# Kernel tuning notes

Measured on AMD Instinct MI355X. Metric: run time of the kernel, lower is better.

The kernel has to match this reference:

```python
import jax, jax.numpy as jnp
import numpy as np

NU, NM = 100000, 20000   # users, merchants
FU, FM = 64, 32          # input feature dims
H = 128                  # hidden_channels
E = 1000000              # edges per edge type
ET = 500000              # target edges


def setup_inputs() -> dict:
    key = jax.random.key(0)
    ks = jax.random.split(key, 24)
    f = lambda i, shape: jax.random.normal(ks[i], shape, jnp.float32) * 0.05
    ri = lambda i, n, hi: jax.random.randint(ks[i], (n,), 0, hi)
    return {
        'x_user': f(0, (NU, FU)),
        'x_merchant': f(1, (NM, FM)),
        'row_um': ri(2, E, NU), 'col_um': ri(3, E, NM),
        'row_mu': ri(4, E, NM), 'col_mu': ri(5, E, NU),
        'row_t': ri(6, ET, NU), 'col_t': ri(7, ET, NM),
        'W1l_um': f(8, (FU, H)), 'W1r_um': f(9, (FM, H)), 'b1_um': jnp.zeros((H,), jnp.float32),
        'W1l_mu': f(10, (FM, H)), 'W1r_mu': f(11, (FU, H)), 'b1_mu': jnp.zeros((H,), jnp.float32),
        'W2l_um': f(12, (H, H)), 'W2r_um': f(13, (H, H)), 'b2_um': jnp.zeros((H,), jnp.float32),
        'W2l_mu': f(14, (H, H)), 'W2r_mu': f(15, (H, H)), 'b2_mu': jnp.zeros((H,), jnp.float32),
        'Wc1': f(16, (2 * H, H)), 'bc1': jnp.zeros((H,), jnp.float32),
        'Wc2': f(17, (H, 1)), 'bc2': jnp.zeros((1,), jnp.float32),
    }


def _sage(x_src, x_dst, row, col, Wl, Wr, b, n_dst):
    # PyG SAGEConv (aggr='mean'): lin_l(mean of neighbor msgs) + lin_r(root) + bias
    deg = jax.ops.segment_sum(jnp.ones(row.shape[0], x_src.dtype), col, num_segments=n_dst)
    agg = jax.ops.segment_sum(x_src[row], col, num_segments=n_dst)
    agg = agg / jnp.maximum(deg, 1.0)[:, None]
    return agg @ Wl + x_dst @ Wr + b


def reference(x_user, x_merchant, row_um, col_um, row_mu, col_mu, row_t, col_t,
              W1l_um, W1r_um, b1_um, W1l_mu, W1r_mu, b1_mu,
              W2l_um, W2r_um, b2_um, W2l_mu, W2r_mu, b2_mu,
              Wc1, bc1, Wc2, bc2):
    # Layer 1 (each dest type receives exactly one edge type -> hetero-mean is identity)
    h_m = jax.nn.relu(_sage(x_user, x_merchant, row_um, col_um, W1l_um, W1r_um, b1_um, NM))
    h_u = jax.nn.relu(_sage(x_merchant, x_user, row_mu, col_mu, W1l_mu, W1r_mu, b1_mu, NU))
    # Layer 2 (no activation)
    z_m = _sage(h_u, h_m, row_um, col_um, W2l_um, W2r_um, b2_um, NM)
    z_u = _sage(h_m, h_u, row_mu, col_mu, W2l_mu, W2r_mu, b2_mu, NU)
    # Edge classifier: gather sender ('user') / receiver ('merchant'), concat, MLP
    z = jnp.concatenate([z_u[row_t], z_m[col_t]], axis=-1)  # [ET, 2H]
    h = jax.nn.relu(z @ Wc1 + bc1)
    return (h @ Wc2 + bc2).reshape(-1)
```

## Files before the change

### kernel.cpp

```cpp
#include <hip/hip_runtime.h>
#include <hip/hip_bf16.h>

#define NUV 100000
#define NMV 20000
#define NEV 1000000
#define ETV 500000

#define CHK 8192
#define NCH 123
#define WNM 5000
#define WNU 25000
#define NCA 5
#define NCB 25
#define HGRID 1954
#define MBLK 5000
#define G1TM 313
#define G2MB 313

typedef unsigned short u16;
typedef unsigned int u32;
typedef __attribute__((ext_vector_type(8))) short s16x8;
typedef __attribute__((ext_vector_type(4))) float f32x4;
typedef __attribute__((ext_vector_type(2))) unsigned int u32x2;
typedef __attribute__((ext_vector_type(4))) unsigned int u32x4;

__device__ inline u16 bf16r(float f) {
  u32 b = __builtin_bit_cast(u32, f);
  u32 r = b + 0x7fffu + ((b >> 16) & 1u);
  return (u16)(r >> 16);
}
__device__ inline float bflo(u32 v) { return __builtin_bit_cast(float, v << 16); }
__device__ inline float bfhi(u32 v) { return __builtin_bit_cast(float, v & 0xffff0000u); }

#define GLOAD_LDS16(src, dst) \
  __builtin_amdgcn_global_load_lds((const __attribute__((address_space(1))) void*)(src), \
                                   (__attribute__((address_space(3))) void*)(dst), 16, 0, 0)

__global__ __launch_bounds__(512) void k_hist_lds(
    const int* __restrict__ col_um, u32* __restrict__ rankp_um, u32* __restrict__ cnt_um,
    const int* __restrict__ col_mu, u32* __restrict__ rankp_mu, u32* __restrict__ cnt_mu) {
  __shared__ u32 hist[WNU];
  int bid = blockIdx.x, tid = threadIdx.x;
  bool um = bid < NCH;
  const int* col = um ? col_um : col_mu;
  u32* rankp = um ? rankp_um : rankp_mu;
  u32* cntp = um ? cnt_um : cnt_mu;
  int Wn = um ? WNM : WNU;
  int blk = um ? bid : bid - NCH;
  int e0 = blk * CHK;
  for (int i = tid; i < Wn; i += 512) hist[i] = 0;
  __syncthreads();
  #pragma unroll
  for (int it = 0; it < CHK / 2048; ++it) {
    int li = e0 + (it * 512 + tid) * 4;
    if (li < NEV) {
      int4 c = *(const int4*)(col + li);
      int cc[4] = {c.x, c.y, c.z, c.w};
      u32 pk = 0;
      #pragma unroll
      for (int q = 0; q < 4; ++q) {
        int d = cc[q];
        int sh = 8 * (d & 3);
        u32 old = atomicAdd(&hist[d >> 2], 1u << sh);
        pk |= ((old >> sh) & 0xFFu) << (8 * q);
      }
      rankp[li >> 2] = pk;
    }
  }
  __syncthreads();
  u32* dst = cntp + (size_t)blk * Wn;
  for (int i = tid; i < Wn; i += 512) dst[i] = hist[i];
}

__global__ __launch_bounds__(1024) void k_scan_s1(
    const u32* __restrict__ cnt_um, u32* __restrict__ pre_um,
    const u32* __restrict__ cnt_mu, u32* __restrict__ pre_mu,
    int* __restrict__ T, int* __restrict__ bsum) {
  int b = blockIdx.x;
  const u32* cnt; u32* pre; int Wn; int w0; int* Tout;
  if (b < NCA) { cnt = cnt_um; pre = pre_um; Wn = WNM; w0 = b * 1024; Tout = T; }
  else         { cnt = cnt_mu; pre = pre_mu; Wn = WNU; w0 = (b - NCA) * 1024; Tout = T + NMV; }
  __shared__ int wsum[16];
  int tid = threadIdx.x, lane = tid & 63, w = tid >> 6;
  int wd = w0 + tid;
  int r0 = 0, r1 = 0, r2 = 0, r3 = 0;
  if (wd < Wn) {
    #pragma unroll 4
    for (int bb = 0; bb < NCH; ++bb) {
      u32 v = cnt[(size_t)bb * Wn + wd];
      pre[(size_t)bb * Wn + wd] =
          (u32)r0 | ((u32)r1 << 8) | ((u32)r2 << 16) | ((u32)r3 << 24);
      r0 += v & 0xFF; r1 += (v >> 8) & 0xFF; r2 += (v >> 16) & 0xFF; r3 += (v >> 24) & 0xFF;
    }
    *(int4*)(Tout + wd * 4) = make_int4(r0, r1, r2, r3);
  }
  int tot = r0 + r1 + r2 + r3;
  #pragma unroll
  for (int d = 1; d < 64; d <<= 1) tot += __shfl_xor(tot, d);
  if (lane == 0) wsum[w] = tot;
  __syncthreads();
  if (tid == 0) {
    int a = 0;
    #pragma unroll
    for (int j = 0; j < 16; ++j) a += wsum[j];
    bsum[b] = a;
  }
}

__global__ __launch_bounds__(128) void k_scan_s2(int* __restrict__ bsum,
                                                 int* __restrict__ off_um, int* __restrict__ off_mu) {
  int tid = threadIdx.x;
  int wv = tid >> 6, lane = tid & 63;
  if (wv == 0) {
    int v = (lane < NCA) ? bsum[lane] : 0;
    int s = v;
    #pragma unroll
    for (int d = 1; d < 64; d <<= 1) { int t = __shfl_up(s, d); if (lane >= d) s += t; }
    if (lane < NCA) bsum[lane] = s - v;
  } else {
    int v = (lane < NCB) ? bsum[NCA + lane] : 0;
    int s = v;
    #pragma unroll
    for (int d = 1; d < 64; d <<= 1) { int t = __shfl_up(s, d); if (lane >= d) s += t; }
    if (lane < NCB) bsum[NCA + lane] = s - v;
  }
  if (tid == 0) { off_um[NMV] = NEV; off_mu[NUV] = NEV; }
}

__global__ __launch_bounds__(1024) void k_scan_s3(int* __restrict__ off_um,
                                                  int* __restrict__ off_mu,
                                                  const int* __restrict__ T,
                                                  const int* __restrict__ bsum) {
  int b = blockIdx.x;
  int N; int c0; int* offo; const int* Tin;
  if (b < NCA) { N = NMV; c0 = b * 4096; offo = off_um; Tin = T; }
  else         { N = NUV; c0 = (b - NCA) * 4096; offo = off_mu; Tin = T + NMV; }
  int carry = bsum[b];
  __shared__ int wsum[16];
  int tid = threadIdx.x, lane = tid & 63, w = tid >> 6;
  int c = c0 + tid * 4;
  int4 tv = make_int4(0, 0, 0, 0);
  if (c < N) tv = *(const int4*)(Tin + c);
  int p1 = tv.x + tv.y, p2 = p1 + tv.z, p3 = p2 + tv.w;
  int sc = p3;
  #pragma unroll
  for (int d = 1; d < 64; d <<= 1) { int t = __shfl_up(sc, d); if (lane >= d) sc += t; }
  if (lane == 63) wsum[w] = sc;
  __syncthreads();
  if (w == 0 && lane < 16) {
    int ws_ = wsum[lane];
    #pragma unroll
    for (int d = 1; d < 16; d <<= 1) { int t = __shfl_up(ws_, d, 16); if (lane >= d) ws_ += t; }
    wsum[lane] = ws_;
  }
  __syncthreads();
  int ex = sc - p3 + (w ? wsum[w - 1] : 0) + carry;
  if (c < N) *(int4*)(offo + c) = make_int4(ex, ex + tv.x, ex + p1, ex + p2);
}

__global__ __launch_bounds__(256) void k_scatter3(
    const int* __restrict__ col_um, const int* __restrict__ row_um,
    const u32* __restrict__ rankp_um, const u32* __restrict__ pre_um,
    const int* __restrict__ off_um, int* __restrict__ srow_um,
    const int* __restrict__ col_mu, const int* __restrict__ row_mu,
    const u32* __restrict__ rankp_mu, const u32* __restrict__ pre_mu,
    const int* __restrict__ off_mu, int* __restrict__ srow_mu) {
  int i = (blockIdx.x * 256 + threadIdx.x) * 4;
  if (i >= 2 * NEV) return;
  bool um = i < NEV;
  const int* col = um ? col_um : col_mu;
  const int* row = um ? row_um : row_mu;
  const u32* rankp = um ? rankp_um : rankp_mu;
  const u32* pre = um ? pre_um : pre_mu;
  const int* off = um ? off_um : off_mu;
  int Wn = um ? WNM : WNU;
  int* srow = um ? srow_um : srow_mu;
  int lo = um ? i : i - NEV;
  int blk = lo >> 13;
  const u32* prep = pre + (size_t)blk * Wn;
  int4 c = *(const int4*)(col + lo);
  int4 rr = *(const int4*)(row + lo);
  u32 pk = rankp[lo >> 2];
  int cc[4] = {c.x, c.y, c.z, c.w}, rv[4] = {rr.x, rr.y, rr.z, rr.w};
  #pragma unroll
  for (int q = 0; q < 4; ++q) {
    int d = cc[q];
    int prefix = (int)((prep[d >> 2] >> (8 * (d & 3))) & 0xFF);
    int rank = (int)((pk >> (8 * q)) & 0xFF);
    srow[off[d] + prefix + rank] = rv[q];
  }
}

__global__ __launch_bounds__(256) void k_prep_w(
    const float* __restrict__ W1l_um, const float* __restrict__ W1r_um,
    const float* __restrict__ W1l_mu, const float* __restrict__ W1r_mu,
    const float* __restrict__ W2l_um, const float* __restrict__ W2r_um,
    const float* __restrict__ W2l_mu, const float* __restrict__ W2r_mu,
    const float* __restrict__ b2_um, const float* __restrict__ b2_mu,
    const float* __restrict__ Wc1, const float* __restrict__ bc1,
    u16* __restrict__ WtA_u, u16* __restrict__ WtB_u,
    u16* __restrict__ WtA_m, u16* __restrict__ WtB_m,
    u16* __restrict__ Wt1_m, u16* __restrict__ Wt1_u,
    float* __restrict__ bias_u, float* __restrict__ bias_m) {
  int t = blockIdx.x * 256 + threadIdx.x;
  if (t < 65536) {
    int mat = t >> 14, rem = t & 16383;
    int o = rem >> 7, k = rem & 127;
    const float* W2 = mat == 0 ? W2l_mu : mat == 1 ? W2r_mu : mat == 2 ? W2l_um : W2r_um;
    const float* wc = Wc1 + (mat >= 2 ? 128 * 128 : 0) + o;
    float s = 0.f;
    #pragma unroll 4
    for (int j = 0; j < 128; ++j) s += W2[k * 128 + j] * wc[j * 128];
    u16* dst = mat == 0 ? WtA_u : mat == 1 ? WtB_u : mat == 2 ? WtA_m : WtB_m;
    dst[o * 128 + k] = bf16r(s);
  } else if (t < 65536 + 256) {
    int r = t - 65536;
    int o = r & 127;
    if (r < 128) {
      float s = 0.f;
      for (int j = 0; j < 128; ++j) s += b2_mu[j] * Wc1[j * 128 + o];
      bias_u[o] = s;
    } else {
      float s = bc1[o];
      for (int j = 0; j < 128; ++j) s += b2_um[j] * Wc1[(128 + j) * 128 + o];
      bias_m[o] = s;
    }
  } else if (t < 65792 + 32768) {
    int idx = t - 65792;
    int mat = idx >> 14, rem = idx & 16383;
    int o = rem >> 7, k = rem & 127;
    if (mat == 0) {
      float v = k < 64 ? W1l_um[k * 128 + o] : (k < 96 ? W1r_um[(k - 64) * 128 + o] : 0.f);
      Wt1_m[o * 128 + k] = bf16r(v);
    } else {
      float v = k < 32 ? W1l_mu[k * 128 + o] : (k < 96 ? W1r_mu[(k - 32) * 128 + o] : 0.f);
      Wt1_u[o * 128 + k] = bf16r(v);
    }
  }
}

__global__ __launch_bounds__(256) void k_prep_x(
    const float* __restrict__ x_user, const float* __restrict__ x_merch,
    u32* __restrict__ cat_u, u32* __restrict__ cat_m) {
  int id = blockIdx.x * 256 + threadIdx.x;
  if (id < NUV * 12) {
    int row = id / 12, wg = id % 12;
    if (wg < 8) {
      const float* src = x_user + (size_t)row * 64 + wg * 8;
      float4 a = *(const float4*)src, b = *(const float4*)(src + 4);
      u32x4 r;
      r[0] = (u32)bf16r(a.x) | ((u32)bf16r(a.y) << 16);
      r[1] = (u32)bf16r(a.z) | ((u32)bf16r(a.w) << 16);
      r[2] = (u32)bf16r(b.x) | ((u32)bf16r(b.y) << 16);
      r[3] = (u32)bf16r(b.z) | ((u32)bf16r(b.w) << 16);
      *(u32x4*)(cat_u + (size_t)row * 64 + 16 + wg * 4) = r;
    } else {
      *(u32x4*)(cat_u + (size_t)row * 64 + 48 + (wg - 8) * 4) = (u32x4){0, 0, 0, 0};
    }
  } else if (id < NUV * 12 + NMV * 8) {
    int id2 = id - NUV * 12;
    int row = id2 / 8, wg = id2 % 8;
    if (wg < 4) {
      const float* src = x_merch + (size_t)row * 32 + wg * 8;
      float4 a = *(const float4*)src, b = *(const float4*)(src + 4);
      u32x4 r;
      r[0] = (u32)bf16r(a.x) | ((u32)bf16r(a.y) << 16);
      r[1] = (u32)bf16r(a.z) | ((u32)bf16r(a.w) << 16);
      r[2] = (u32)bf16r(b.x) | ((u32)bf16r(b.y) << 16);
      r[3] = (u32)bf16r(b.z) | ((u32)bf16r(b.w) << 16);
      *(u32x4*)(cat_m + (size_t)row * 64 + 32 + wg * 4) = r;
    } else {
      *(u32x4*)(cat_m + (size_t)row * 64 + 48 + (wg - 4) * 4) = (u32x4){0, 0, 0, 0};
    }
  }
}

__global__ __launch_bounds__(256) void k_agg_l1(
    const int* __restrict__ off_um, const int* __restrict__ srow_um,
    const int* __restrict__ off_mu, const int* __restrict__ srow_mu,
    u32* __restrict__ cat_u, u32* __restrict__ cat_m) {
  int bid = blockIdx.x, tid = threadIdx.x;
  int l = tid & 63, g = l >> 3, lr = l & 7;
  if (bid < MBLK) {
    int wid = (bid * 256 + tid) >> 6;
    int s = off_um[wid], t = off_um[wid + 1];
    const u32* gx = cat_u;
    float a[8] = {};
    int j = s;
    for (; j + 32 <= t; j += 32) {
      int r0 = srow_um[j + g], r1 = srow_um[j + 8 + g];
      int r2 = srow_um[j + 16 + g], r3 = srow_um[j + 24 + g];
      u32x4 v0 = *(const u32x4*)(gx + (size_t)r0 * 64 + 16 + lr * 4);
      u32x4 v1 = *(const u32x4*)(gx + (size_t)r1 * 64 + 16 + lr * 4);
      u32x4 v2 = *(const u32x4*)(gx + (size_t)r2 * 64 + 16 + lr * 4);
      u32x4 v3 = *(const u32x4*)(gx + (size_t)r3 * 64 + 16 + lr * 4);
      #pragma unroll
      for (int k = 0; k < 4; ++k) {
        a[2 * k] += (bflo(v0[k]) + bflo(v1[k])) + (bflo(v2[k]) + bflo(v3[k]));
        a[2 * k + 1] += (bfhi(v0[k]) + bfhi(v1[k])) + (bfhi(v2[k]) + bfhi(v3[k]));
      }
    }
    for (; j + 8 <= t; j += 8) {
      int r0 = srow_um[j + g];
      u32x4 v0 = *(const u32x4*)(gx + (size_t)r0 * 64 + 16 + lr * 4);
      #pragma unroll
      for (int k = 0; k < 4; ++k) { a[2 * k] += bflo(v0[k]); a[2 * k + 1] += bfhi(v0[k]); }
    }
    if (g < t - j) {
      int r0 = srow_um[j + g];
      u32x4 v0 = *(const u32x4*)(gx + (size_t)r0 * 64 + 16 + lr * 4);
      #pragma unroll
      for (int k = 0; k < 4; ++k) { a[2 * k] += bflo(v0[k]); a[2 * k + 1] += bfhi(v0[k]); }
    }
    #pragma unroll
    for (int k = 0; k < 8; ++k) {
      a[k] += __shfl_xor(a[k], 8);
      a[k] += __shfl_xor(a[k], 16);
      a[k] += __shfl_xor(a[k], 32);
    }
    if (g == 0) {
      float inv = 1.f / (float)max(t - s, 1);
      u32x4 o;
      #pragma unroll
      for (int k = 0; k < 4; ++k)
        o[k] = (u32)bf16r(a[2 * k] * inv) | ((u32)bf16r(a[2 * k + 1] * inv) << 16);
      *(u32x4*)(cat_m + (size_t)wid * 64 + lr * 4) = o;
    }
  } else {
    int wid = ((bid - MBLK) * 256 + tid) >> 6;
    int s = off_mu[wid], t = off_mu[wid + 1];
    const u32* gx = cat_m;
    float a[4] = {};
    int j = s;
    for (; j + 32 <= t; j += 32) {
      int r0 = srow_mu[j + g], r1 = srow_mu[j + 8 + g];
      int r2 = srow_mu[j + 16 + g], r3 = srow_mu[j + 24 + g];
      u32x2 v0 = *(const u32x2*)(gx + (size_t)r0 * 64 + 32 + lr * 2);
      u32x2 v1 = *(const u32x2*)(gx + (size_t)r1 * 64 + 32 + lr * 2);
      u32x2 v2 = *(const u32x2*)(gx + (size_t)r2 * 64 + 32 + lr * 2);
      u32x2 v3 = *(const u32x2*)(gx + (size_t)r3 * 64 + 32 + lr * 2);
      #pragma unroll
      for (int k = 0; k < 2; ++k) {
        a[2 * k] += (bflo(v0[k]) + bflo(v1[k])) + (bflo(v2[k]) + bflo(v3[k]));
        a[2 * k + 1] += (bfhi(v0[k]) + bfhi(v1[k])) + (bfhi(v2[k]) + bfhi(v3[k]));
      }
    }
    for (; j + 8 <= t; j += 8) {
      int r0 = srow_mu[j + g];
      u32x2 v0 = *(const u32x2*)(gx + (size_t)r0 * 64 + 32 + lr * 2);
      #pragma unroll
      for (int k = 0; k < 2; ++k) { a[2 * k] += bflo(v0[k]); a[2 * k + 1] += bfhi(v0[k]); }
    }
    if (g < t - j) {
      int r0 = srow_mu[j + g];
      u32x2 v0 = *(const u32x2*)(gx + (size_t)r0 * 64 + 32 + lr * 2);
      #pragma unroll
      for (int k = 0; k < 2; ++k) { a[2 * k] += bflo(v0[k]); a[2 * k + 1] += bfhi(v0[k]); }
    }
    #pragma unroll
    for (int k = 0; k < 4; ++k) {
      a[k] += __shfl_xor(a[k], 8);
      a[k] += __shfl_xor(a[k], 16);
      a[k] += __shfl_xor(a[k], 32);
    }
    if (g == 0) {
      float inv = 1.f / (float)max(t - s, 1);
      u32x2 o;
      #pragma unroll
      for (int k = 0; k < 2; ++k)
        o[k] = (u32)bf16r(a[2 * k] * inv) | ((u32)bf16r(a[2 * k + 1] * inv) << 16);
      *(u32x2*)(cat_u + (size_t)wid * 64 + lr * 2) = o;
    }
  }
}

__global__ __launch_bounds__(256) void k_gemm1_mfma(
    const u16* __restrict__ cat_m, const u16* __restrict__ Wt1_m,
    const float* __restrict__ b1_um, u16* __restrict__ h_m,
    const u16* __restrict__ cat_u, const u16* __restrict__ Wt1_u,
    const float* __restrict__ b1_mu, u16* __restrict__ h_u) {
  __shared__ u16 Zs[64 * 128];
  int tid = threadIdx.x, bid = blockIdx.x;
  const u16 *cat, *Wt; const float* bias; u16* ho; int nd, r0;
  if (bid < G1TM) { cat = cat_m; Wt = Wt1_m; bias = b1_um; ho = h_m; nd = NMV; r0 = bid * 64; }
  else { cat = cat_u; Wt = Wt1_u; bias = b1_mu; ho = h_u; nd = NUV; r0 = (bid - G1TM) * 64; }
  #pragma unroll
  for (int it = 0; it < 4; ++it) {
    int q = tid + it * 256;
    int rl = q >> 4;
    int cc = (q & 15) ^ (rl & 7);
    int r = r0 + rl; r = r < nd ? r : nd - 1;
    const u16* src = cat + (size_t)r * 128 + cc * 8;
    u16* dst = Zs + (tid >> 6) * 512 + it * 2048;
    GLOAD_LDS16(src, dst);
  }
  __syncthreads();
  int l = tid & 63, wv = tid >> 6;
  int lg = l >> 4, lr = l & 15;
  f32x4 acc[4][2];
  #pragma unroll
  for (int mt = 0; mt < 4; ++mt)
    #pragma unroll
    for (int c = 0; c < 2; ++c) acc[mt][c] = (f32x4){0.f, 0.f, 0.f, 0.f};
  #pragma unroll
  for (int cti = 0; cti < 2; ++cti) {
    int o = (wv * 2 + cti) * 16 + lr;
    const u16* wp = Wt + (size_t)o * 128 + lg * 8;
    s16x8 b[4];
    #pragma unroll
    for (int ks = 0; ks < 4; ++ks) b[ks] = *(const s16x8*)(wp + ks * 32);
    #pragma unroll
    for (int mt = 0; mt < 4; ++mt) {
      int rl = mt * 16 + lr;
      int rb = rl * 256, sw = (rl & 7) << 4;
      #pragma unroll
      for (int ks = 0; ks < 4; ++ks) {
        s16x8 a = *(const s16x8*)((const char*)Zs + ((rb + ks * 64 + lg * 16) ^ sw));
        acc[mt][cti] = __builtin_amdgcn_mfma_f32_16x16x32_bf16(a, b[ks], acc[mt][cti], 0, 0, 0);
      }
    }
  }
  float bv[2];
  #pragma unroll
  for (int cti = 0; cti < 2; ++cti) bv[cti] = bias[(wv * 2 + cti) * 16 + lr];
  #pragma unroll
  for (int mt = 0; mt < 4; ++mt)
    #pragma unroll
    for (int cti = 0; cti < 2; ++cti) {
      int o = (wv * 2 + cti) * 16 + lr;
      #pragma unroll
      for (int rg = 0; rg < 4; ++rg) {
        int r = r0 + mt * 16 + lg * 4 + rg;
        if (r < nd) {
          float v = acc[mt][cti][rg] + bv[cti];
          v = v > 0.f ? v : 0.f;
          ho[(size_t)r * 128 + o] = bf16r(v);
        }
      }
    }
}

__global__ __launch_bounds__(256) void k_agg_l2(
    const int* __restrict__ off_um, const int* __restrict__ srow_um,
    const u16* __restrict__ h_u, u16* __restrict__ aggb_m,
    const int* __restrict__ off_mu, const int* __restrict__ srow_mu,
    const u16* __restrict__ h_m, u16* __restrict__ aggb_u) {
  int bid = blockIdx.x, tid = threadIdx.x;
  const int* off; const int* srow; const u32* x; u32* ag; int wid;
  if (bid < MBLK) {
    off = off_um; srow = srow_um; x = (const u32*)h_u; ag = (u32*)aggb_m;
    wid = (bid * 256 + tid) >> 6;
  } else {
    off = off_mu; srow = srow_mu; x = (const u32*)h_m; ag = (u32*)aggb_u;
    wid = ((bid - MBLK) * 256 + tid) >> 6;
  }
  int l = tid & 63, g = l >> 4, lr = l & 15;
  int s = off[wid], t = off[wid + 1];
  float a[8] = {};
  int j = s;
  for (; j + 16 <= t; j += 16) {
    int r0 = srow[j + g], r1 = srow[j + 4 + g];
    int r2 = srow[j + 8 + g], r3 = srow[j + 12 + g];
    u32x4 v0 = *(const u32x4*)(x + (size_t)r0 * 64 + lr * 4);
    u32x4 v1 = *(const u32x4*)(x + (size_t)r1 * 64 + lr * 4);
    u32x4 v2 = *(const u32x4*)(x + (size_t)r2 * 64 + lr * 4);
    u32x4 v3 = *(const u32x4*)(x + (size_t)r3 * 64 + lr * 4);
    #pragma unroll
    for (int k = 0; k < 4; ++k) {
      a[2 * k] += (bflo(v0[k]) + bflo(v1[k])) + (bflo(v2[k]) + bflo(v3[k]));
      a[2 * k + 1] += (bfhi(v0[k]) + bfhi(v1[k])) + (bfhi(v2[k]) + bfhi(v3[k]));
    }
  }
  for (; j + 4 <= t; j += 4) {
    int r0 = srow[j + g];
    u32x4 v0 = *(const u32x4*)(x + (size_t)r0 * 64 + lr * 4);
    #pragma unroll
    for (int k = 0; k < 4; ++k) { a[2 * k] += bflo(v0[k]); a[2 * k + 1] += bfhi(v0[k]); }
  }
  if (g < t - j) {
    int r0 = srow[j + g];
    u32x4 v0 = *(const u32x4*)(x + (size_t)r0 * 64 + lr * 4);
    #pragma unroll
    for (int k = 0; k < 4; ++k) { a[2 * k] += bflo(v0[k]); a[2 * k + 1] += bfhi(v0[k]); }
  }
  #pragma unroll
  for (int k = 0; k < 8; ++k) {
    a[k] += __shfl_xor(a[k], 16);
    a[k] += __shfl_xor(a[k], 32);
  }
  if (g == 0) {
    float inv = 1.f / (float)max(t - s, 1);
    u32x4 o;
    #pragma unroll
    for (int k = 0; k < 4; ++k)
      o[k] = (u32)bf16r(a[2 * k] * inv) | ((u32)bf16r(a[2 * k + 1] * inv) << 16);
    *(u32x4*)(ag + (size_t)wid * 64 + lr * 4) = o;
  }
}

__global__ __launch_bounds__(256) void k_gemm2_mfma(
    const u16* __restrict__ aggb_m, const u16* __restrict__ h_m,
    const u16* __restrict__ WtA_m, const u16* __restrict__ WtB_m,
    const float* __restrict__ bias_m, u16* __restrict__ pm_b,
    const u16* __restrict__ aggb_u, const u16* __restrict__ h_u,
    const u16* __restrict__ WtA_u, const u16* __restrict__ WtB_u,
    const float* __restrict__ bias_u, u16* __restrict__ pu_b) {
  __shared__ u16 Zs[64 * 256];
  int tid = threadIdx.x;
  int bid = blockIdx.x;
  const u16 *aggb, *hb, *Wtl, *Wtr; const float* bias; u16* zb; int nd, r0;
  if (bid < G2MB) {
    aggb = aggb_m; hb = h_m; Wtl = WtA_m; Wtr = WtB_m; bias = bias_m; zb = pm_b;
    nd = NMV; r0 = bid * 64;
  } else {
    aggb = aggb_u; hb = h_u; Wtl = WtA_u; Wtr = WtB_u; bias = bias_u; zb = pu_b;
    nd = NUV; r0 = (bid - G2MB) * 64;
  }
  {
    int half = (tid >> 4) & 1;
    const u16* tab = half ? hb : aggb;
    #pragma unroll
    for (int it = 0; it < 8; ++it) {
      int q = tid + it * 256;
      int rl = q >> 5;
      int cc = (q & 15) ^ (rl & 7);
      int r = r0 + rl; r = r < nd ? r : nd - 1;
      const u16* src = tab + (size_t)r * 128 + cc * 8;
      u16* dst = Zs + (tid >> 6) * 512 + it * 2048;
      GLOAD_LDS16(src, dst);
    }
  }
  __syncthreads();
  int l = tid & 63, wv = tid >> 6;
  int lg = l >> 4, lr = l & 15;
  f32x4 acc[4][2];
  #pragma unroll
  for (int mt = 0; mt < 4; ++mt)
    #pragma unroll
    for (int c = 0; c < 2; ++c) acc[mt][c] = (f32x4){0.f, 0.f, 0.f, 0.f};
  #pragma unroll
  for (int cti = 0; cti < 2; ++cti) {
    int o = (wv * 2 + cti) * 16 + lr;
    const u16* wpl = Wtl + (size_t)o * 128 + lg * 8;
    const u16* wpr = Wtr + (size_t)o * 128 + lg * 8;
    s16x8 b[8];
    #pragma unroll
    for (int ks = 0; ks < 4; ++ks) b[ks] = *(const s16x8*)(wpl + ks * 32);
    #pragma unroll
    for (int ks = 0; ks < 4; ++ks) b[ks + 4] = *(const s16x8*)(wpr + ks * 32);
    #pragma unroll
    for (int mt = 0; mt < 4; ++mt) {
      int rl = mt * 16 + lr;
      int rb = rl * 512, sw = (rl & 7) << 4;
      #pragma unroll
      for (int ks = 0; ks < 8; ++ks) {
        s16x8 a = *(const s16x8*)((const char*)Zs + ((rb + ks * 64 + lg * 16) ^ sw));
        acc[mt][cti] = __builtin_amdgcn_mfma_f32_16x16x32_bf16(a, b[ks], acc[mt][cti], 0, 0, 0);
      }
    }
  }
  float bv[2];
  #pragma unroll
  for (int cti = 0; cti < 2; ++cti) bv[cti] = bias[(wv * 2 + cti) * 16 + lr];
  #pragma unroll
  for (int mt = 0; mt < 4; ++mt)
    #pragma unroll
    for (int cti = 0; cti < 2; ++cti) {
      int o = (wv * 2 + cti) * 16 + lr;
      #pragma unroll
      for (int rg = 0; rg < 4; ++rg) {
        int r = r0 + mt * 16 + lg * 4 + rg;
        if (r < nd) zb[(size_t)r * 128 + o] = bf16r(acc[mt][cti][rg] + bv[cti]);
      }
    }
}

__global__ __launch_bounds__(256) void k_edge(
    const u32* __restrict__ pu, const u32* __restrict__ pm,
    const int* __restrict__ row_t, const int* __restrict__ col_t,
    const float* __restrict__ Wc2, const float* __restrict__ bc2,
    float* __restrict__ out) {
  __shared__ float res[256];
  int tid = threadIdx.x, l = tid & 63, wv = tid >> 6;
  int lr = l & 15, g = l >> 4;
  float w2v[8];
  #pragma unroll
  for (int q = 0; q < 8; ++q) w2v[q] = Wc2[lr * 8 + q];
  int base = blockIdx.x * 256 + wv * 64;
  #pragma unroll 2
  for (int it = 0; it < 16; ++it) {
    int e = base + it * 4 + g;
    int ec = e < ETV ? e : ETV - 1;
    int r = row_t[ec], c = col_t[ec];
    u32x4 a = *(const u32x4*)(pu + (size_t)r * 64 + lr * 4);
    u32x4 b = *(const u32x4*)(pm + (size_t)c * 64 + lr * 4);
    float p = 0.f;
    #pragma unroll
    for (int q = 0; q < 4; ++q) {
      float h0 = bflo(a[q]) + bflo(b[q]);
      float h1 = bfhi(a[q]) + bfhi(b[q]);
      h0 = h0 > 0.f ? h0 : 0.f;
      h1 = h1 > 0.f ? h1 : 0.f;
      p += h0 * w2v[2 * q] + h1 * w2v[2 * q + 1];
    }
    p += __shfl_xor(p, 1); p += __shfl_xor(p, 2);
    p += __shfl_xor(p, 4); p += __shfl_xor(p, 8);
    if (lr == 0) res[wv * 64 + it * 4 + g] = p;
  }
  __syncthreads();
  int eo = blockIdx.x * 256 + tid;
  if (eo < ETV) out[eo] = res[tid] + bc2[0];
}

extern "C" void kernel_launch(void* const* d_in, const int* in_sizes, int n_in,
                              void* d_out, int out_size, void* d_ws, size_t ws_size,
                              hipStream_t stream) {
  const float* x_user  = (const float*)d_in[0];
  const float* x_merch = (const float*)d_in[1];
  const int* row_um = (const int*)d_in[2]; const int* col_um = (const int*)d_in[3];
  const int* row_mu = (const int*)d_in[4]; const int* col_mu = (const int*)d_in[5];
  const int* row_t  = (const int*)d_in[6]; const int* col_t  = (const int*)d_in[7];
  const float* W1l_um = (const float*)d_in[8];  const float* W1r_um = (const float*)d_in[9];  const float* b1_um = (const float*)d_in[10];
  const float* W1l_mu = (const float*)d_in[11]; const float* W1r_mu = (const float*)d_in[12]; const float* b1_mu = (const float*)d_in[13];
  const float* W2l_um = (const float*)d_in[14]; const float* W2r_um = (const float*)d_in[15]; const float* b2_um = (const float*)d_in[16];
  const float* W2l_mu = (const float*)d_in[17]; const float* W2r_mu = (const float*)d_in[18]; const float* b2_mu = (const float*)d_in[19];
  const float* Wc1 = (const float*)d_in[20]; const float* bc1 = (const float*)d_in[21];
  const float* Wc2 = (const float*)d_in[22]; const float* bc2 = (const float*)d_in[23];
  float* out = (float*)d_out;

  char* ws = (char*)d_ws;
  size_t p = 0;
  auto alloc = [&](size_t bytes) -> char* {
    char* r = ws + p;
    p = (p + bytes + 255) & ~(size_t)255;
    return r;
  };
  u32* cnt_um = (u32*)alloc((size_t)NCH * WNM * 4);
  u32* cnt_mu = (u32*)alloc((size_t)NCH * WNU * 4);
  u32* pre_um = (u32*)alloc((size_t)NCH * WNM * 4);
  u32* pre_mu = (u32*)alloc((size_t)NCH * WNU * 4);
  u32* rankp_um = (u32*)alloc((size_t)(NEV / 4) * 4);
  u32* rankp_mu = (u32*)alloc((size_t)(NEV / 4) * 4);
  int* off_um = (int*)alloc((size_t)(NMV + 4) * 4);
  int* off_mu = (int*)alloc((size_t)(NUV + 4) * 4);
  int* T    = (int*)alloc((size_t)(NMV + NUV) * 4);
  int* bsum = (int*)alloc((size_t)(NCA + NCB) * 4);
  int* srow_um = (int*)alloc((size_t)NEV * 4);
  int* srow_mu = (int*)alloc((size_t)NEV * 4);
  u16* cat_m = (u16*)alloc((size_t)NMV * 128 * 2);
  u16* cat_u = (u16*)alloc((size_t)NUV * 128 * 2);
  u16* h_m   = (u16*)alloc((size_t)NMV * 128 * 2);
  u16* h_u   = (u16*)alloc((size_t)NUV * 128 * 2);
  u16* aggb_m = (u16*)alloc((size_t)NMV * 128 * 2);
  u16* aggb_u = (u16*)alloc((size_t)NUV * 128 * 2);
  u16* pm_b  = (u16*)alloc((size_t)NMV * 128 * 2);
  u16* pu_b  = (u16*)alloc((size_t)NUV * 128 * 2);
  u16* WtA_u = (u16*)alloc((size_t)128 * 128 * 2);
  u16* WtB_u = (u16*)alloc((size_t)128 * 128 * 2);
  u16* WtA_m = (u16*)alloc((size_t)128 * 128 * 2);
  u16* WtB_m = (u16*)alloc((size_t)128 * 128 * 2);
  u16* Wt1_m = (u16*)alloc((size_t)128 * 128 * 2);
  u16* Wt1_u = (u16*)alloc((size_t)128 * 128 * 2);
  float* bias_u = (float*)alloc(128 * 4);
  float* bias_m = (float*)alloc(128 * 4);
  if (p > ws_size) return;

  k_prep_w<<<386, 256, 0, stream>>>(W1l_um, W1r_um, W1l_mu, W1r_mu,
                                    W2l_um, W2r_um, W2l_mu, W2r_mu, b2_um, b2_mu, Wc1, bc1,
                                    WtA_u, WtB_u, WtA_m, WtB_m, Wt1_m, Wt1_u, bias_u, bias_m);
  k_prep_x<<<(NUV * 12 + NMV * 8 + 255) / 256, 256, 0, stream>>>(x_user, x_merch,
                                                                 (u32*)cat_u, (u32*)cat_m);
  k_hist_lds<<<2 * NCH, 512, 0, stream>>>(col_um, rankp_um, cnt_um,
                                          col_mu, rankp_mu, cnt_mu);
  k_scan_s1<<<NCA + NCB, 1024, 0, stream>>>(cnt_um, pre_um, cnt_mu, pre_mu, T, bsum);
  k_scan_s2<<<1, 128, 0, stream>>>(bsum, off_um, off_mu);
  k_scan_s3<<<NCA + NCB, 1024, 0, stream>>>(off_um, off_mu, T, bsum);
  k_scatter3<<<HGRID, 256, 0, stream>>>(col_um, row_um, rankp_um, pre_um, off_um, srow_um,
                                        col_mu, row_mu, rankp_mu, pre_mu, off_mu, srow_mu);
  k_agg_l1<<<MBLK + NUV / 4, 256, 0, stream>>>(off_um, srow_um, off_mu, srow_mu,
                                               (u32*)cat_u, (u32*)cat_m);
  k_gemm1_mfma<<<G1TM + (NUV + 63) / 64, 256, 0, stream>>>(cat_m, Wt1_m, b1_um, h_m,
                                                           cat_u, Wt1_u, b1_mu, h_u);
  k_agg_l2<<<MBLK + NUV / 4, 256, 0, stream>>>(off_um, srow_um, h_u, aggb_m,
                                               off_mu, srow_mu, h_m, aggb_u);
  k_gemm2_mfma<<<G2MB + (NUV + 63) / 64, 256, 0, stream>>>(
      aggb_m, h_m, WtA_m, WtB_m, bias_m, pm_b,
      aggb_u, h_u, WtA_u, WtB_u, bias_u, pu_b);
  k_edge<<<(ETV + 255) / 256, 256, 0, stream>>>((const u32*)pu_b, (const u32*)pm_b,
                                                row_t, col_t, Wc2, bc2, out);
}
```

Measured before the change: 322.5 us.

## Fuse layer-2 mean aggregation into the GEMM and merge prep and scan launches

Layer-2 neighbour mean aggregation now runs inside the layer-2 MFMA GEMM kernel. Each block gathers and averages its 64 destination rows straight into LDS, which removes the aggb intermediate buffers and their global write and read-back. The weight-prep and feature-prep kernels are merged into one launch. The tiny scan_s2 kernel is dropped, and each scan_s3 block now sums the block totals it needs on its own. The cost is far less gather parallelism in the fused kernel: one wave handles 16 rows in sequence instead of one row per wave, so gather latency may be hidden less well.

```diff
diff --git a/kernel.cpp b/kernel.cpp
--- a/kernel.cpp
+++ b/kernel.cpp
@@ -16,6 +16,7 @@
 #define MBLK 5000
 #define G1TM 313
 #define G2MB 313
+#define PWB 386
 
 typedef unsigned short u16;
 typedef unsigned int u32;
@@ -107,26 +108,6 @@
   }
 }
 
-__global__ __launch_bounds__(128) void k_scan_s2(int* __restrict__ bsum,
-                                                 int* __restrict__ off_um, int* __restrict__ off_mu) {
-  int tid = threadIdx.x;
-  int wv = tid >> 6, lane = tid & 63;
-  if (wv == 0) {
-    int v = (lane < NCA) ? bsum[lane] : 0;
-    int s = v;
-    #pragma unroll
-    for (int d = 1; d < 64; d <<= 1) { int t = __shfl_up(s, d); if (lane >= d) s += t; }
-    if (lane < NCA) bsum[lane] = s - v;
-  } else {
-    int v = (lane < NCB) ? bsum[NCA + lane] : 0;
-    int s = v;
-    #pragma unroll
-    for (int d = 1; d < 64; d <<= 1) { int t = __shfl_up(s, d); if (lane >= d) s += t; }
-    if (lane < NCB) bsum[NCA + lane] = s - v;
-  }
-  if (tid == 0) { off_um[NMV] = NEV; off_mu[NUV] = NEV; }
-}
-
 __global__ __launch_bounds__(1024) void k_scan_s3(int* __restrict__ off_um,
                                                   int* __restrict__ off_mu,
                                                   const int* __restrict__ T,
@@ -135,9 +116,18 @@
   int N; int c0; int* offo; const int* Tin;
   if (b < NCA) { N = NMV; c0 = b * 4096; offo = off_um; Tin = T; }
   else         { N = NUV; c0 = (b - NCA) * 4096; offo = off_mu; Tin = T + NMV; }
-  int carry = bsum[b];
+  __shared__ int carry_s;
   __shared__ int wsum[16];
   int tid = threadIdx.x, lane = tid & 63, w = tid >> 6;
+  if (tid == 0) {
+    int lo = (b < NCA) ? 0 : NCA;
+    int c = 0;
+    for (int j = lo; j < b; ++j) c += bsum[j];
+    carry_s = c;
+    if (b == 0) { off_um[NMV] = NEV; off_mu[NUV] = NEV; }
+  }
+  __syncthreads();
+  int carry = carry_s;
   int c = c0 + tid * 4;
   int4 tv = make_int4(0, 0, 0, 0);
   if (c < N) tv = *(const int4*)(Tin + c);
@@ -191,7 +181,8 @@
   }
 }
 
-__global__ __launch_bounds__(256) void k_prep_w(
+__global__ __launch_bounds__(256) void k_prep(
+    const float* __restrict__ x_user, const float* __restrict__ x_merch,
     const float* __restrict__ W1l_um, const float* __restrict__ W1r_um,
     const float* __restrict__ W1l_mu, const float* __restrict__ W1r_mu,
     const float* __restrict__ W2l_um, const float* __restrict__ W2r_um,
@@ -201,76 +192,76 @@
     u16* __restrict__ WtA_u, u16* __restrict__ WtB_u,
     u16* __restrict__ WtA_m, u16* __restrict__ WtB_m,
     u16* __restrict__ Wt1_m, u16* __restrict__ Wt1_u,
-    float* __restrict__ bias_u, float* __restrict__ bias_m) {
-  int t = blockIdx.x * 256 + threadIdx.x;
-  if (t < 65536) {
-    int mat = t >> 14, rem = t & 16383;
-    int o = rem >> 7, k = rem & 127;
-    const float* W2 = mat == 0 ? W2l_mu : mat == 1 ? W2r_mu : mat == 2 ? W2l_um : W2r_um;
-    const float* wc = Wc1 + (mat >= 2 ? 128 * 128 : 0) + o;
-    float s = 0.f;
-    #pragma unroll 4
-    for (int j = 0; j < 128; ++j) s += W2[k * 128 + j] * wc[j * 128];
-    u16* dst = mat == 0 ? WtA_u : mat == 1 ? WtB_u : mat == 2 ? WtA_m : WtB_m;
-    dst[o * 128 + k] = bf16r(s);
-  } else if (t < 65536 + 256) {
-    int r = t - 65536;
-    int o = r & 127;
-    if (r < 128) {
+    float* __restrict__ bias_u, float* __restrict__ bias_m,
+    u32* __restrict__ cat_u, u32* __restrict__ cat_m) {
+  int bid = blockIdx.x;
+  if (bid < PWB) {
+    int t = bid * 256 + threadIdx.x;
+    if (t < 65536) {
+      int mat = t >> 14, rem = t & 16383;
+      int o = rem >> 7, k = rem & 127;
+      const float* W2 = mat == 0 ? W2l_mu : mat == 1 ? W2r_mu : mat == 2 ? W2l_um : W2r_um;
+      const float* wc = Wc1 + (mat >= 2 ? 128 * 128 : 0) + o;
       float s = 0.f;
-      for (int j = 0; j < 128; ++j) s += b2_mu[j] * Wc1[j * 128 + o];
-      bias_u[o] = s;
-    } else {
-      float s = bc1[o];
-      for (int j = 0; j < 128; ++j) s += b2_um[j] * Wc1[(128 + j) * 128 + o];
-      bias_m[o] = s;
-    }
-  } else if (t < 65792 + 32768) {
-    int idx = t - 65792;
-    int mat = idx >> 14, rem = idx & 16383;
-    int o = rem >> 7, k = rem & 127;
-    if (mat == 0) {
-      float v = k < 64 ? W1l_um[k * 128 + o] : (k < 96 ? W1r_um[(k - 64) * 128 + o] : 0.f);
-      Wt1_m[o * 128 + k] = bf16r(v);
-    } else {
-      float v = k < 32 ? W1l_mu[k * 128 + o] : (k < 96 ? W1r_mu[(k - 32) * 128 + o] : 0.f);
-      Wt1_u[o * 128 + k] = bf16r(v);
-    }
-  }
-}
-
-__global__ __launch_bounds__(256) void k_prep_x(
-    const float* __restrict__ x_user, const float* __restrict__ x_merch,
-    u32* __restrict__ cat_u, u32* __restrict__ cat_m) {
-  int id = blockIdx.x * 256 + threadIdx.x;
-  if (id < NUV * 12) {
-    int row = id / 12, wg = id % 12;
-    if (wg < 8) {
-      const float* src = x_user + (size_t)row * 64 + wg * 8;
-      float4 a = *(const float4*)src, b = *(const float4*)(src + 4);
-      u32x4 r;
-      r[0] = (u32)bf16r(a.x) | ((u32)bf16r(a.y) << 16);
-      r[1] = (u32)bf16r(a.z) | ((u32)bf16r(a.w) << 16);
-      r[2] = (u32)bf16r(b.x) | ((u32)bf16r(b.y) << 16);
-      r[3] = (u32)bf16r(b.z) | ((u32)bf16r(b.w) << 16);
-      *(u32x4*)(cat_u + (size_t)row * 64 + 16 + wg * 4) = r;
-    } else {
-      *(u32x4*)(cat_u + (size_t)row * 64 + 48 + (wg - 8) * 4) = (u32x4){0, 0, 0, 0};
-    }
-  } else if (id < NUV * 12 + NMV * 8) {
-    int id2 = id - NUV * 12;
-    int row = id2 / 8, wg = id2 % 8;
-    if (wg < 4) {
-      const float* src = x_merch + (size_t)row * 32 + wg * 8;
-      float4 a = *(const float4*)src, b = *(const float4*)(src + 4);
-      u32x4 r;
-      r[0] = (u32)bf16r(a.x) | ((u32)bf16r(a.y) << 16);
-      r[1] = (u32)bf16r(a.z) | ((u32)bf16r(a.w) << 16);
-      r[2] = (u32)bf16r(b.x) | ((u32)bf16r(b.y) << 16);
-      r[3] = (u32)bf16r(b.z) | ((u32)bf16r(b.w) << 16);
-      *(u32x4*)(cat_m + (size_t)row * 64 + 32 + wg * 4) = r;
-    } else {
-      *(u32x4*)(cat_m + (size_t)row * 64 + 48 + (wg - 4) * 4) = (u32x4){0, 0, 0, 0};
+      #pragma unroll 4
+      for (int j = 0; j < 128; ++j) s += W2[k * 128 + j] * wc[j * 128];
+      u16* dst = mat == 0 ? WtA_u : mat == 1 ? WtB_u : mat == 2 ? WtA_m : WtB_m;
+      dst[o * 128 + k] = bf16r(s);
+    } else if (t < 65536 + 256) {
+      int r = t - 65536;
+      int o = r & 127;
+      if (r < 128) {
+        float s = 0.f;
+        for (int j = 0; j < 128; ++j) s += b2_mu[j] * Wc1[j * 128 + o];
+        bias_u[o] = s;
+      } else {
+        float s = bc1[o];
+        for (int j = 0; j < 128; ++j) s += b2_um[j] * Wc1[(128 + j) * 128 + o];
+        bias_m[o] = s;
+      }
+    } else if (t < 65792 + 32768) {
+      int idx = t - 65792;
+      int mat = idx >> 14, rem = idx & 16383;
+      int o = rem >> 7, k = rem & 127;
+      if (mat == 0) {
+        float v = k < 64 ? W1l_um[k * 128 + o] : (k < 96 ? W1r_um[(k - 64) * 128 + o] : 0.f);
+        Wt1_m[o * 128 + k] = bf16r(v);
+      } else {
+        float v = k < 32 ? W1l_mu[k * 128 + o] : (k < 96 ? W1r_mu[(k - 32) * 128 + o] : 0.f);
+        Wt1_u[o * 128 + k] = bf16r(v);
+      }
+    }
+  } else {
+    int id = (bid - PWB) * 256 + threadIdx.x;
+    if (id < NUV * 12) {
+      int row = id / 12, wg = id % 12;
+      if (wg < 8) {
+        const float* src = x_user + (size_t)row * 64 + wg * 8;
+        float4 a = *(const float4*)src, b = *(const float4*)(src + 4);
+        u32x4 r;
+        r[0] = (u32)bf16r(a.x) | ((u32)bf16r(a.y) << 16);
+        r[1] = (u32)bf16r(a.z) | ((u32)bf16r(a.w) << 16);
+        r[2] = (u32)bf16r(b.x) | ((u32)bf16r(b.y) << 16);
+        r[3] = (u32)bf16r(b.z) | ((u32)bf16r(b.w) << 16);
+        *(u32x4*)(cat_u + (size_t)row * 64 + 16 + wg * 4) = r;
+      } else {
+        *(u32x4*)(cat_u + (size_t)row * 64 + 48 + (wg - 8) * 4) = (u32x4){0, 0, 0, 0};
+      }
+    } else if (id < NUV * 12 + NMV * 8) {
+      int id2 = id - NUV * 12;
+      int row = id2 / 8, wg = id2 % 8;
+      if (wg < 4) {
+        const float* src = x_merch + (size_t)row * 32 + wg * 8;
+        float4 a = *(const float4*)src, b = *(const float4*)(src + 4);
+        u32x4 r;
+        r[0] = (u32)bf16r(a.x) | ((u32)bf16r(a.y) << 16);
+        r[1] = (u32)bf16r(a.z) | ((u32)bf16r(a.w) << 16);
+        r[2] = (u32)bf16r(b.x) | ((u32)bf16r(b.y) << 16);
+        r[3] = (u32)bf16r(b.z) | ((u32)bf16r(b.w) << 16);
+        *(u32x4*)(cat_m + (size_t)row * 64 + 32 + wg * 4) = r;
+      } else {
+        *(u32x4*)(cat_m + (size_t)row * 64 + 48 + (wg - 4) * 4) = (u32x4){0, 0, 0, 0};
+      }
     }
   }
 }
@@ -440,99 +431,85 @@
     }
 }
 
-__global__ __launch_bounds__(256) void k_agg_l2(
+__global__ __launch_bounds__(256) void k_gemm2f(
     const int* __restrict__ off_um, const int* __restrict__ srow_um,
-    const u16* __restrict__ h_u, u16* __restrict__ aggb_m,
     const int* __restrict__ off_mu, const int* __restrict__ srow_mu,
-    const u16* __restrict__ h_m, u16* __restrict__ aggb_u) {
-  int bid = blockIdx.x, tid = threadIdx.x;
-  const int* off; const int* srow; const u32* x; u32* ag; int wid;
-  if (bid < MBLK) {
-    off = off_um; srow = srow_um; x = (const u32*)h_u; ag = (u32*)aggb_m;
-    wid = (bid * 256 + tid) >> 6;
-  } else {
-    off = off_mu; srow = srow_mu; x = (const u32*)h_m; ag = (u32*)aggb_u;
-    wid = ((bid - MBLK) * 256 + tid) >> 6;
-  }
-  int l = tid & 63, g = l >> 4, lr = l & 15;
-  int s = off[wid], t = off[wid + 1];
-  float a[8] = {};
-  int j = s;
-  for (; j + 16 <= t; j += 16) {
-    int r0 = srow[j + g], r1 = srow[j + 4 + g];
-    int r2 = srow[j + 8 + g], r3 = srow[j + 12 + g];
-    u32x4 v0 = *(const u32x4*)(x + (size_t)r0 * 64 + lr * 4);
-    u32x4 v1 = *(const u32x4*)(x + (size_t)r1 * 64 + lr * 4);
-    u32x4 v2 = *(const u32x4*)(x + (size_t)r2 * 64 + lr * 4);
-    u32x4 v3 = *(const u32x4*)(x + (size_t)r3 * 64 + lr * 4);
-    #pragma unroll
-    for (int k = 0; k < 4; ++k) {
-      a[2 * k] += (bflo(v0[k]) + bflo(v1[k])) + (bflo(v2[k]) + bflo(v3[k]));
-      a[2 * k + 1] += (bfhi(v0[k]) + bfhi(v1[k])) + (bfhi(v2[k]) + bfhi(v3[k]));
-    }
-  }
-  for (; j + 4 <= t; j += 4) {
-    int r0 = srow[j + g];
-    u32x4 v0 = *(const u32x4*)(x + (size_t)r0 * 64 + lr * 4);
-    #pragma unroll
-    for (int k = 0; k < 4; ++k) { a[2 * k] += bflo(v0[k]); a[2 * k + 1] += bfhi(v0[k]); }
-  }
-  if (g < t - j) {
-    int r0 = srow[j + g];
-    u32x4 v0 = *(const u32x4*)(x + (size_t)r0 * 64 + lr * 4);
-    #pragma unroll
-    for (int k = 0; k < 4; ++k) { a[2 * k] += bflo(v0[k]); a[2 * k + 1] += bfhi(v0[k]); }
-  }
-  #pragma unroll
-  for (int k = 0; k < 8; ++k) {
-    a[k] += __shfl_xor(a[k], 16);
-    a[k] += __shfl_xor(a[k], 32);
-  }
-  if (g == 0) {
-    float inv = 1.f / (float)max(t - s, 1);
-    u32x4 o;
-    #pragma unroll
-    for (int k = 0; k < 4; ++k)
-      o[k] = (u32)bf16r(a[2 * k] * inv) | ((u32)bf16r(a[2 * k + 1] * inv) << 16);
-    *(u32x4*)(ag + (size_t)wid * 64 + lr * 4) = o;
-  }
-}
-
-__global__ __launch_bounds__(256) void k_gemm2_mfma(
-    const u16* __restrict__ aggb_m, const u16* __restrict__ h_m,
+    const u16* __restrict__ h_m, const u16* __restrict__ h_u,
     const u16* __restrict__ WtA_m, const u16* __restrict__ WtB_m,
     const float* __restrict__ bias_m, u16* __restrict__ pm_b,
-    const u16* __restrict__ aggb_u, const u16* __restrict__ h_u,
     const u16* __restrict__ WtA_u, const u16* __restrict__ WtB_u,
     const float* __restrict__ bias_u, u16* __restrict__ pu_b) {
-  __shared__ u16 Zs[64 * 256];
-  int tid = threadIdx.x;
-  int bid = blockIdx.x;
-  const u16 *aggb, *hb, *Wtl, *Wtr; const float* bias; u16* zb; int nd, r0;
+  __shared__ u16 Zh[64 * 128];
+  __shared__ u16 Za[64 * 128];
+  int tid = threadIdx.x, bid = blockIdx.x;
+  const int *off, *srow; const u32* gtab; const u16 *hb, *Wtl, *Wtr;
+  const float* bias; u16* zb; int nd, r0;
   if (bid < G2MB) {
-    aggb = aggb_m; hb = h_m; Wtl = WtA_m; Wtr = WtB_m; bias = bias_m; zb = pm_b;
-    nd = NMV; r0 = bid * 64;
+    off = off_um; srow = srow_um; gtab = (const u32*)h_u; hb = h_m;
+    Wtl = WtA_m; Wtr = WtB_m; bias = bias_m; zb = pm_b; nd = NMV; r0 = bid * 64;
   } else {
-    aggb = aggb_u; hb = h_u; Wtl = WtA_u; Wtr = WtB_u; bias = bias_u; zb = pu_b;
-    nd = NUV; r0 = (bid - G2MB) * 64;
-  }
-  {
-    int half = (tid >> 4) & 1;
-    const u16* tab = half ? hb : aggb;
-    #pragma unroll
-    for (int it = 0; it < 8; ++it) {
-      int q = tid + it * 256;
-      int rl = q >> 5;
-      int cc = (q & 15) ^ (rl & 7);
-      int r = r0 + rl; r = r < nd ? r : nd - 1;
-      const u16* src = tab + (size_t)r * 128 + cc * 8;
-      u16* dst = Zs + (tid >> 6) * 512 + it * 2048;
-      GLOAD_LDS16(src, dst);
-    }
-  }
-  __syncthreads();
+    off = off_mu; srow = srow_mu; gtab = (const u32*)h_m; hb = h_u;
+    Wtl = WtA_u; Wtr = WtB_u; bias = bias_u; zb = pu_b; nd = NUV; r0 = (bid - G2MB) * 64;
+  }
+  #pragma unroll
+  for (int it = 0; it < 4; ++it) {
+    int q = tid + it * 256;
+    int rl = q >> 4;
+    int cc = (q & 15) ^ (rl & 7);
+    int r = r0 + rl; r = r < nd ? r : nd - 1;
+    GLOAD_LDS16(hb + (size_t)r * 128 + cc * 8, Zh + (tid >> 6) * 512 + it * 2048);
+  }
   int l = tid & 63, wv = tid >> 6;
-  int lg = l >> 4, lr = l & 15;
+  int g = l >> 4, lr = l & 15;
+  for (int i = 0; i < 16; ++i) {
+    int rl = wv * 16 + i;
+    int r = r0 + rl;
+    bool ok = r < nd;
+    int s = ok ? off[r] : 0, t = ok ? off[r + 1] : 0;
+    float a[8] = {};
+    int j = s;
+    for (; j + 16 <= t; j += 16) {
+      int r0e = srow[j + g], r1e = srow[j + 4 + g];
+      int r2e = srow[j + 8 + g], r3e = srow[j + 12 + g];
+      u32x4 v0 = *(const u32x4*)(gtab + (size_t)r0e * 64 + lr * 4);
+      u32x4 v1 = *(const u32x4*)(gtab + (size_t)r1e * 64 + lr * 4);
+      u32x4 v2 = *(const u32x4*)(gtab + (size_t)r2e * 64 + lr * 4);
+      u32x4 v3 = *(const u32x4*)(gtab + (size_t)r3e * 64 + lr * 4);
+      #pragma unroll
+      for (int k = 0; k < 4; ++k) {
+        a[2 * k] += (bflo(v0[k]) + bflo(v1[k])) + (bflo(v2[k]) + bflo(v3[k]));
+        a[2 * k + 1] += (bfhi(v0[k]) + bfhi(v1[k])) + (bfhi(v2[k]) + bfhi(v3[k]));
+      }
+    }
+    for (; j + 4 <= t; j += 4) {
+      int r0e = srow[j + g];
+      u32x4 v0 = *(const u32x4*)(gtab + (size_t)r0e * 64 + lr * 4);
+      #pragma unroll
+      for (int k = 0; k < 4; ++k) { a[2 * k] += bflo(v0[k]); a[2 * k + 1] += bfhi(v0[k]); }
+    }
+    if (g < t - j) {
+      int r0e = srow[j + g];
+      u32x4 v0 = *(const u32x4*)(gtab + (size_t)r0e * 64 + lr * 4);
+      #pragma unroll
+      for (int k = 0; k < 4; ++k) { a[2 * k] += bflo(v0[k]); a[2 * k + 1] += bfhi(v0[k]); }
+    }
+    #pragma unroll
+    for (int k = 0; k < 8; ++k) {
+      a[k] += __shfl_xor(a[k], 16);
+      a[k] += __shfl_xor(a[k], 32);
+    }
+    if (g == 0) {
+      float inv = 1.f / (float)max(t - s, 1);
+      u32x4 o;
+      #pragma unroll
+      for (int k = 0; k < 4; ++k)
+        o[k] = ok ? ((u32)bf16r(a[2 * k] * inv) | ((u32)bf16r(a[2 * k + 1] * inv) << 16)) : 0u;
+      int byt = (rl * 256 + lr * 16) ^ ((rl & 7) << 4);
+      *(u32x4*)((char*)Za + byt) = o;
+    }
+  }
+  __syncthreads();
+  int lg = g;
   f32x4 acc[4][2];
   #pragma unroll
   for (int mt = 0; mt < 4; ++mt)
@@ -551,11 +528,16 @@
     #pragma unroll
     for (int mt = 0; mt < 4; ++mt) {
       int rl = mt * 16 + lr;
-      int rb = rl * 512, sw = (rl & 7) << 4;
-      #pragma unroll
-      for (int ks = 0; ks < 8; ++ks) {
-        s16x8 a = *(const s16x8*)((const char*)Zs + ((rb + ks * 64 + lg * 16) ^ sw));
+      int rb = rl * 256, sw = (rl & 7) << 4;
+      #pragma unroll
+      for (int ks = 0; ks < 4; ++ks) {
+        s16x8 a = *(const s16x8*)((const char*)Za + ((rb + ks * 64 + lg * 16) ^ sw));
         acc[mt][cti] = __builtin_amdgcn_mfma_f32_16x16x32_bf16(a, b[ks], acc[mt][cti], 0, 0, 0);
+      }
+      #pragma unroll
+      for (int ks = 0; ks < 4; ++ks) {
+        s16x8 a = *(const s16x8*)((const char*)Zh + ((rb + ks * 64 + lg * 16) ^ sw));
+        acc[mt][cti] = __builtin_amdgcn_mfma_f32_16x16x32_bf16(a, b[ks + 4], acc[mt][cti], 0, 0, 0);
       }
     }
   }
@@ -651,8 +633,6 @@
   u16* cat_u = (u16*)alloc((size_t)NUV * 128 * 2);
   u16* h_m   = (u16*)alloc((size_t)NMV * 128 * 2);
   u16* h_u   = (u16*)alloc((size_t)NUV * 128 * 2);
-  u16* aggb_m = (u16*)alloc((size_t)NMV * 128 * 2);
-  u16* aggb_u = (u16*)alloc((size_t)NUV * 128 * 2);
   u16* pm_b  = (u16*)alloc((size_t)NMV * 128 * 2);
   u16* pu_b  = (u16*)alloc((size_t)NUV * 128 * 2);
   u16* WtA_u = (u16*)alloc((size_t)128 * 128 * 2);
@@ -665,15 +645,14 @@
   float* bias_m = (float*)alloc(128 * 4);
   if (p > ws_size) return;
 
-  k_prep_w<<<386, 256, 0, stream>>>(W1l_um, W1r_um, W1l_mu, W1r_mu,
-                                    W2l_um, W2r_um, W2l_mu, W2r_mu, b2_um, b2_mu, Wc1, bc1,
-                                    WtA_u, WtB_u, WtA_m, WtB_m, Wt1_m, Wt1_u, bias_u, bias_m);
-  k_prep_x<<<(NUV * 12 + NMV * 8 + 255) / 256, 256, 0, stream>>>(x_user, x_merch,
-                                                                 (u32*)cat_u, (u32*)cat_m);
+  k_prep<<<PWB + (NUV * 12 + NMV * 8 + 255) / 256, 256, 0, stream>>>(
+      x_user, x_merch, W1l_um, W1r_um, W1l_mu, W1r_mu,
+      W2l_um, W2r_um, W2l_mu, W2r_mu, b2_um, b2_mu, Wc1, bc1,
+      WtA_u, WtB_u, WtA_m, WtB_m, Wt1_m, Wt1_u, bias_u, bias_m,
+      (u32*)cat_u, (u32*)cat_m);
   k_hist_lds<<<2 * NCH, 512, 0, stream>>>(col_um, rankp_um, cnt_um,
                                           col_mu, rankp_mu, cnt_mu);
   k_scan_s1<<<NCA + NCB, 1024, 0, stream>>>(cnt_um, pre_um, cnt_mu, pre_mu, T, bsum);
-  k_scan_s2<<<1, 128, 0, stream>>>(bsum, off_um, off_mu);
   k_scan_s3<<<NCA + NCB, 1024, 0, stream>>>(off_um, off_mu, T, bsum);
   k_scatter3<<<HGRID, 256, 0, stream>>>(col_um, row_um, rankp_um, pre_um, off_um, srow_um,
                                         col_mu, row_mu, rankp_mu, pre_mu, off_mu, srow_mu);
@@ -681,11 +660,9 @@
                                                (u32*)cat_u, (u32*)cat_m);
   k_gemm1_mfma<<<G1TM + (NUV + 63) / 64, 256, 0, stream>>>(cat_m, Wt1_m, b1_um, h_m,
                                                            cat_u, Wt1_u, b1_mu, h_u);
-  k_agg_l2<<<MBLK + NUV / 4, 256, 0, stream>>>(off_um, srow_um, h_u, aggb_m,
-                                               off_mu, srow_mu, h_m, aggb_u);
-  k_gemm2_mfma<<<G2MB + (NUV + 63) / 64, 256, 0, stream>>>(
-      aggb_m, h_m, WtA_m, WtB_m, bias_m, pm_b,
-      aggb_u, h_u, WtA_u, WtB_u, bias_u, pu_b);
+  k_gemm2f<<<G2MB + (NUV + 63) / 64, 256, 0, stream>>>(
+      off_um, srow_um, off_mu, srow_mu, h_m, h_u,
+      WtA_m, WtB_m, bias_m, pm_b, WtA_u, WtB_u, bias_u, pu_b);
   k_edge<<<(ETV + 255) / 256, 256, 0, stream>>>((const u32*)pu_b, (const u32*)pm_b,
                                                 row_t, col_t, Wc2, bc2, out);
 }
```

Measured after the change: 410.8 us. +27.4%, slower.
